# Optimization experiments

Measured on AMD Instinct MI355X. Metric: run time of the kernel, lower is better.

Reference implementation:

```python
import jax, jax.numpy as jnp
import numpy as np

B, L, D, H, C = 16, 512, 1280, 512, 5


def setup_inputs() -> dict:
    key = jax.random.key(0)
    ks = jax.random.split(key, 20)
    emb = jax.random.normal(ks[0], (B, L, D), jnp.float32)
    lengths = jax.random.randint(ks[1], (B,), 16, L + 1)
    attention_mask = (jnp.arange(L)[None, :] < lengths[:, None]).astype(jnp.int32)
    sc = 1.0 / np.sqrt(H)
    u = lambda k, s: jax.random.uniform(k, s, jnp.float32, -sc, sc)
    return dict(
        embeddings=emb,
        attention_mask=attention_mask,
        h0=jax.random.normal(ks[2], (2, B, H), jnp.float32),
        c0=jax.random.normal(ks[3], (2, B, H), jnp.float32),
        w_ih_f=u(ks[4], (4 * H, D)), w_hh_f=u(ks[5], (4 * H, H)),
        b_ih_f=u(ks[6], (4 * H,)), b_hh_f=u(ks[7], (4 * H,)),
        w_ih_b=u(ks[8], (4 * H, D)), w_hh_b=u(ks[9], (4 * H, H)),
        b_ih_b=u(ks[10], (4 * H,)), b_hh_b=u(ks[11], (4 * H,)),
        w_out=u(ks[12], (2 * H, C)), b_out=u(ks[13], (C,)),
        crf_start=jax.random.normal(ks[14], (C,), jnp.float32) * 0.1,
        crf_end=jax.random.normal(ks[15], (C,), jnp.float32) * 0.1,
        crf_trans=jax.random.normal(ks[16], (C, C), jnp.float32) * 0.1,
    )


def _lstm_dir(x, h0, c0, w_ih, w_hh, b_ih, b_hh):
    # x: [B, T, D] -> hidden states [B, T, H]; PyTorch gate order (i, f, g, o)
    xg = jnp.einsum('btd,gd->btg', x, w_ih) + b_ih + b_hh  # [B, T, 4H]

    def step(carry, xw_t):
        h, c = carry
        g = xw_t + h @ w_hh.T
        i, f, gg, o = jnp.split(g, 4, axis=-1)
        c = jax.nn.sigmoid(f) * c + jax.nn.sigmoid(i) * jnp.tanh(gg)
        h = jax.nn.sigmoid(o) * jnp.tanh(c)
        return (h, c), h

    _, hs = jax.lax.scan(step, (h0, c0), xg.transpose(1, 0, 2))
    return hs.transpose(1, 0, 2)


def _emissions(embeddings, attention_mask, h0, c0, w_ih_f, w_hh_f, b_ih_f, b_hh_f,
               w_ih_b, w_hh_b, b_ih_b, b_hh_b, w_out, b_out):
    lengths = attention_mask.sum(axis=1)
    x = embeddings[:, 1:-1]                                   # drop CLS position, shift left
    Tp = x.shape[1]
    valid = jnp.arange(Tp)[None, :] < (lengths - 2)[:, None]  # remove_cls crop [1:len-1], left-aligned pad
    x = jnp.where(valid[:, :, None], x, 0.0)
    hf = _lstm_dir(x, h0[0], c0[0], w_ih_f, w_hh_f, b_ih_f, b_hh_f)
    hb = _lstm_dir(x[:, ::-1], h0[1], c0[1], w_ih_b, w_hh_b, b_ih_b, b_hh_b)[:, ::-1]
    h = jnp.concatenate([hf, hb], axis=-1)                    # [B, Tp, 2H]
    return h @ w_out + b_out, valid


def _viterbi_decode(emissions, mask, start, end, trans):
    Bn, Tp, Ct = emissions.shape
    ident = jnp.arange(Ct, dtype=jnp.int32)
    score0 = start[None, :] + emissions[:, 0]                 # [B, C]

    def step(score, inp):
        emit_t, m_t = inp                                      # [B, C], [B]
        br = score[:, :, None] + trans[None] + emit_t[:, None, :]
        ns = br.max(axis=1)
        idx = br.argmax(axis=1).astype(jnp.int32)
        idx = jnp.where(m_t[:, None], idx, ident[None, :])     # identity backpointer past seq end
        score = jnp.where(m_t[:, None], ns, score)
        return score, idx

    score, hist = jax.lax.scan(step, score0,
                               (emissions[:, 1:].transpose(1, 0, 2), mask[:, 1:].T))
    score = score + end[None, :]
    last = jnp.argmax(score, axis=-1).astype(jnp.int32)        # [B]
    bidx = jnp.arange(Bn)

    def bstep(tag, idx_t):
        prev = idx_t[bidx, tag]
        return prev, prev

    _, prevs = jax.lax.scan(bstep, last, hist, reverse=True)   # [Tp-1, B]
    tags = jnp.concatenate([prevs, last[None, :]], axis=0).transpose(1, 0)
    return tags


def reference(embeddings, attention_mask, h0, c0, w_ih_f, w_hh_f, b_ih_f, b_hh_f,
              w_ih_b, w_hh_b, b_ih_b, b_hh_b, w_out, b_out, crf_start, crf_end, crf_trans):
    emissions, valid = _emissions(embeddings, attention_mask, h0, c0,
                                  w_ih_f, w_hh_f, b_ih_f, b_hh_f,
                                  w_ih_b, w_hh_b, b_ih_b, b_hh_b, w_out, b_out)
    tags = _viterbi_decode(emissions, valid, crf_start, crf_end, crf_trans)
    return tags, valid  # tags valid where mask True (past-end entries repeat last tag)
```

## Files before the change

kernel.cpp:

```cpp
#include <hip/hip_runtime.h>

typedef unsigned short u16;
typedef unsigned int u32;
typedef __bf16 bf16x8 __attribute__((ext_vector_type(8)));
typedef u16 u16x8 __attribute__((ext_vector_type(8)));
typedef float f32x4 __attribute__((ext_vector_type(4)));
typedef u32 u32x2 __attribute__((ext_vector_type(2)));
typedef u32 u32x4 __attribute__((ext_vector_type(4)));

#define B_ 16
#define T_ 510
#define H_ 512
#define N_ 4096
#define KSPLIT 2560

#define OFF_ABIG  0ull
#define OFF_BBIG  41943040ull
#define OFF_BIAS  62914560ull
#define OFF_XG    62930944ull
#define OFF_HS    197148672ull
#define OFF_EMIS  230572032ull
#define OFF_V     230735232ull
#define OFF_FLAGS 230735296ull
#define OFF_PROBE  (OFF_EMIS + 131328ull)
#define OFF_CTRL   (OFF_EMIS + 131584ull)
#define CHUNKA_OFF 0ull
#define CHUNKB_OFF 262144ull

#define MAGIC_ 0x5EC0FFEE
#define POLL_BUDGET 65536
#define ARB_BUDGET  262144

#define GL_LDS(g, s) __builtin_amdgcn_global_load_lds(                      \
    (const __attribute__((address_space(1))) void*)(g),                     \
    (__attribute__((address_space(3))) void*)(s), 16, 0, 0)

__device__ __forceinline__ u16 f2bf(float x) {
  u32 u = __float_as_uint(x);
  u32 r = (u + 0x7fffu + ((u >> 16) & 1u)) >> 16;
  return (u16)r;
}
__device__ __forceinline__ float bf2f(u16 h) { return __uint_as_float(((u32)h) << 16); }

__device__ __forceinline__ int ld_cc(const int* p) {
  int f;
  asm volatile("global_load_dword %0, %1, off sc0 sc1\n\ts_waitcnt vmcnt(0)" : "=v"(f) : "v"(p) : "memory");
  return f;
}
__device__ __forceinline__ void st_cc(int* p, int v) {
  asm volatile("global_store_dword %0, %1, off sc0 sc1\n\ts_waitcnt vmcnt(0)" :: "v"(p), "v"(v) : "memory");
}

__device__ __forceinline__ float sigm_f(float x) {
  float e = __expf(-x);
  return __builtin_amdgcn_rcpf(1.f + e);
}
__device__ __forceinline__ float tanh_f(float x) {
  float e = __expf(2.f * x);
  return 1.f - 2.f * __builtin_amdgcn_rcpf(e + 1.f);
}

__global__ __launch_bounds__(256) void k_prep(const int* __restrict__ mask, int* __restrict__ V,
                                              int* __restrict__ flagsA, int* __restrict__ probe,
                                              int* __restrict__ ctrl) {
  __shared__ int red[4];
  int b = blockIdx.x, tid = threadIdx.x;
  int s = mask[b * 512 + tid] + mask[b * 512 + 256 + tid];
  for (int off = 32; off; off >>= 1) s += __shfl_down(s, off);
  if ((tid & 63) == 0) red[tid >> 6] = s;
  __syncthreads();
  if (tid == 0) V[b] = red[0] + red[1] + red[2] + red[3] - 2;
  if (b == 0 && tid < 64) flagsA[tid] = 0;
  if (b == 3 && tid < 64) probe[tid] = 0;
  if (b == 1 && tid < 16) ctrl[tid] = 0;
}

__global__ __launch_bounds__(256) void k_zero(char* __restrict__ p) {
  u32x4 z = (u32x4){0u, 0u, 0u, 0u};
  char* dst = p + ((size_t)blockIdx.x * 256 + threadIdx.x) * 16;
  asm volatile("global_store_dwordx4 %0, %1, off sc0 sc1" :: "v"(dst), "v"(z) : "memory");
}

__global__ __launch_bounds__(256) void k_valid(const int* __restrict__ V, int* __restrict__ out) {
  int idx = blockIdx.x * 256 + threadIdx.x;
  if (idx < B_ * T_) {
    int b = idx / T_, t = idx - b * T_;
    out[B_ * T_ + idx] = (t < V[b]) ? 1 : 0;
  }
}

__global__ __launch_bounds__(320) void k_splitA(const float* __restrict__ emb, const int* __restrict__ V,
                                                u16* __restrict__ Abig) {
  int row = blockIdx.x;
  int k0 = threadIdx.x * 4;
  u16* dst = Abig + (size_t)row * KSPLIT;
  float4 v = {0.f, 0.f, 0.f, 0.f};
  if (row < B_ * T_) {
    int b = row / T_, t = row - b * T_;
    if (t < V[b]) v = *(const float4*)(emb + (size_t)(b * 512 + t + 1) * 1280 + k0);
  }
  float vs[4] = {v.x, v.y, v.z, v.w};
  ushort4 hi, lo;
  u16 h0_ = f2bf(vs[0]); u16 l0_ = f2bf(vs[0] - bf2f(h0_));
  u16 h1_ = f2bf(vs[1]); u16 l1_ = f2bf(vs[1] - bf2f(h1_));
  u16 h2_ = f2bf(vs[2]); u16 l2_ = f2bf(vs[2] - bf2f(h2_));
  u16 h3_ = f2bf(vs[3]); u16 l3_ = f2bf(vs[3] - bf2f(h3_));
  hi.x = h0_; hi.y = h1_; hi.z = h2_; hi.w = h3_;
  lo.x = l0_; lo.y = l1_; lo.z = l2_; lo.w = l3_;
  *(ushort4*)(dst + k0) = hi;
  *(ushort4*)(dst + 1280 + k0) = lo;
}

__global__ __launch_bounds__(320) void k_splitB(const float* __restrict__ wf, const float* __restrict__ wb,
                                                const float* __restrict__ bihf, const float* __restrict__ bhhf,
                                                const float* __restrict__ bihb, const float* __restrict__ bhhb,
                                                u16* __restrict__ Bbig, float* __restrict__ bias) {
  int n = blockIdx.x;
  int k0 = threadIdx.x * 4;
  int d = n >> 11, g = n & 2047;
  const float* w = (d ? wb : wf) + (size_t)g * 1280;
  float4 v = *(const float4*)(w + k0);
  float vs[4] = {v.x, v.y, v.z, v.w};
  ushort4 hi, lo;
  u16 h0_ = f2bf(vs[0]); u16 l0_ = f2bf(vs[0] - bf2f(h0_));
  u16 h1_ = f2bf(vs[1]); u16 l1_ = f2bf(vs[1] - bf2f(h1_));
  u16 h2_ = f2bf(vs[2]); u16 l2_ = f2bf(vs[2] - bf2f(h2_));
  u16 h3_ = f2bf(vs[3]); u16 l3_ = f2bf(vs[3] - bf2f(h3_));
  hi.x = h0_; hi.y = h1_; hi.z = h2_; hi.w = h3_;
  lo.x = l0_; lo.y = l1_; lo.z = l2_; lo.w = l3_;
  u16* dst = Bbig + (size_t)n * KSPLIT;
  *(ushort4*)(dst + k0) = hi;
  *(ushort4*)(dst + 1280 + k0) = lo;
  if (threadIdx.x == 0) bias[n] = d ? (bihb[g] + bhhb[g]) : (bihf[g] + bhhf[g]);
}

__global__ __launch_bounds__(256, 2) void k_gemm(const u16* __restrict__ A, const u16* __restrict__ Bt,
                                                 const float* __restrict__ bias, float* __restrict__ C) {
  __shared__ __align__(16) u16 As[128 * 64];
  __shared__ __align__(16) u16 Bs[128 * 64];
  const int tid = threadIdx.x;
  const int w = tid >> 6, l = tid & 63;
  const int wm = w >> 1, wn = w & 1;
  const int bm = blockIdx.x, bn = blockIdx.y;
  f32x4 acc[4][4];
#pragma unroll
  for (int m = 0; m < 4; ++m)
#pragma unroll
    for (int n = 0; n < 4; ++n) acc[m][n] = (f32x4){0.f, 0.f, 0.f, 0.f};

  const int rQ = tid >> 3;
  const int cB = (tid & 7) * 16;
  const char* gA = (const char*)(A + (size_t)(bm * 128) * KSPLIT) + cB;
  const char* gB = (const char*)(Bt + (size_t)(bn * 128) * KSPLIT) + cB;

  for (int kt = 0; kt < 60; ++kt) {
    const int s = kt / 20, ks = kt - s * 20;
    const int aOff = ((s == 2) ? 1280 : 0) + ks * 64;
    const int bOff = ((s == 1) ? 1280 : 0) + ks * 64;
    __syncthreads();
#pragma unroll
    for (int q = 0; q < 4; ++q) {
      GL_LDS(gA + ((size_t)(q * 32 + rQ) * KSPLIT + aOff) * 2, (char*)As + q * 4096 + tid * 16);
      GL_LDS(gB + ((size_t)(q * 32 + rQ) * KSPLIT + bOff) * 2, (char*)Bs + q * 4096 + tid * 16);
    }
    __syncthreads();
#pragma unroll
    for (int kc = 0; kc < 2; ++kc) {
      bf16x8 af[4], bfr[4];
      const int kByte = kc * 64 + (l >> 4) * 16;
#pragma unroll
      for (int m = 0; m < 4; ++m)
        af[m] = *(const bf16x8*)((const char*)As + (wm * 64 + m * 16 + (l & 15)) * 128 + kByte);
#pragma unroll
      for (int n = 0; n < 4; ++n)
        bfr[n] = *(const bf16x8*)((const char*)Bs + (wn * 64 + n * 16 + (l & 15)) * 128 + kByte);
#pragma unroll
      for (int m = 0; m < 4; ++m)
#pragma unroll
        for (int n = 0; n < 4; ++n)
          acc[m][n] = __builtin_amdgcn_mfma_f32_16x16x32_bf16(af[m], bfr[n], acc[m][n], 0, 0, 0);
    }
  }
#pragma unroll
  for (int n = 0; n < 4; ++n) {
    const int gc = bn * 128 + wn * 64 + n * 16 + (l & 15);
    const float bv = bias[gc];
#pragma unroll
    for (int m = 0; m < 4; ++m) {
      const int gr0 = bm * 128 + wm * 64 + m * 16 + (l >> 4) * 4;
#pragma unroll
      for (int r = 0; r < 4; ++r) C[(size_t)(gr0 + r) * N_ + gc] = acc[m][n][r] + bv;
    }
  }
}

template <int COH>
__device__ __forceinline__ void emit_chunks(char* buf, int sub, u32 gen, const u16* pack) {
  const int tid = threadIdx.x;
  if (tid < 128) {
    const int sb = tid >> 3, r = tid & 7, p = r >> 2, j = r & 3;
    const u32* pw = (const u32*)(pack + p * 256 + sb * 16 + j * 4);
    u32x4 val;
    val[0] = pw[0]; val[1] = pw[1]; val[2] = gen; val[3] = 0u;
    char* dst = buf + sb * 4096 + p * 2048 + (sub * 4 + j) * 16;
    if constexpr (COH)
      asm volatile("global_store_dwordx4 %0, %1, off" :: "v"(dst), "v"(val) : "memory");
    else
      asm volatile("global_store_dwordx4 %0, %1, off sc0 sc1" :: "v"(dst), "v"(val) : "memory");
  }
}

template <int COH>
__device__ void run_recur(int dir, int sub, const float* __restrict__ xg, const float* __restrict__ whh,
                          const float* __restrict__ h0, const float* __restrict__ c0,
                          float* __restrict__ hs, char* __restrict__ cb,
                          u16* lds_a, float* epil, u16* pack) {
  const int tid = threadIdx.x;
  const int w = tid >> 6, l = tid & 63;
  const int c = l & 15, kg = l >> 4;
  const int gate = c >> 2, uloc = c & 3;
  const int ug = sub * 16 + w * 4 + uloc;

  __syncthreads();

  bf16x8 whi[16], wlo[16];
  {
    const float* wrow = whh + (size_t)(gate * 512 + ug) * 512 + kg * 8;
#pragma unroll
    for (int kc = 0; kc < 16; ++kc) {
      float4 v0 = *(const float4*)(wrow + kc * 32);
      float4 v1 = *(const float4*)(wrow + kc * 32 + 4);
      float vs[8] = {v0.x, v0.y, v0.z, v0.w, v1.x, v1.y, v1.z, v1.w};
      u16x8 hi, lo;
#pragma unroll
      for (int j = 0; j < 8; ++j) {
        u16 h = f2bf(vs[j]);
        hi[j] = h;
        lo[j] = f2bf(vs[j] - bf2f(h));
      }
      whi[kc] = __builtin_bit_cast(bf16x8, hi);
      wlo[kc] = __builtin_bit_cast(bf16x8, lo);
    }
  }

  const int sb = tid >> 4, su = tid & 15;
  const int gu = sub * 16 + su;
  float creg = c0[(dir * 16 + sb) * 512 + gu];
  {
    float h = h0[(dir * 16 + sb) * 512 + gu];
    u16 hh = f2bf(h), hl = f2bf(h - bf2f(hh));
    pack[sb * 16 + su] = hh;
    pack[256 + sb * 16 + su] = hl;
  }
  __syncthreads();
  emit_chunks<COH>(cb + 65536, sub, 1u, pack);

  for (int t = 0; t < T_; ++t) {
    const int trow = dir ? (T_ - 1 - t) : t;
    const u32 gen = (u32)(t + 1);
    const char* sbuf = cb + ((t + 1) & 1) * 65536;

    u32x4 v[16];
#pragma unroll
    for (int i = 0; i < 16; ++i) {
      const char* p = sbuf + ((size_t)(tid + 256 * i)) * 16;
      asm volatile("global_load_dwordx4 %0, %1, off sc0 sc1" : "=v"(v[i]) : "v"(p) : "memory");
    }
    float xv[4];
#pragma unroll
    for (int g = 0; g < 4; ++g) {
      const float* p = xg + (size_t)(sb * T_ + trow) * N_ + dir * 2048 + g * 512 + gu;
      asm volatile("global_load_dword %0, %1, off" : "=v"(xv[g]) : "v"(p) : "memory");
    }
    asm volatile("s_waitcnt vmcnt(4)" ::: "memory");
    __builtin_amdgcn_sched_barrier(0);
    while (true) {
      u32 bad = 0;
#pragma unroll
      for (int i = 0; i < 16; ++i) bad |= (v[i][2] != gen) ? (1u << i) : 0u;
      if (!bad) break;
#pragma unroll
      for (int i = 0; i < 16; ++i)
        if (bad & (1u << i)) {
          const char* p = sbuf + ((size_t)(tid + 256 * i)) * 16;
          asm volatile("global_load_dwordx4 %0, %1, off sc0 sc1" : "=v"(v[i]) : "v"(p) : "memory");
        }
      asm volatile("s_waitcnt vmcnt(0)" ::: "memory");
      __builtin_amdgcn_sched_barrier(0);
    }
#pragma unroll
    for (int i = 0; i < 16; ++i) {
      int ci = tid + 256 * i;
      int b = ci >> 8, pl = (ci >> 7) & 1, k = ci & 127;
      int off = pl * 16384 + b * 1024 + ((k * 8) ^ ((b & 7) << 4));
      *(u32x2*)((char*)lds_a + off) = (u32x2){v[i][0], v[i][1]};
    }
    __syncthreads();

    f32x4 a0 = (f32x4){0.f, 0.f, 0.f, 0.f}, a1 = a0, a2 = a0, a3 = a0, a4 = a0, a5 = a0;
#pragma unroll
    for (int kc = 0; kc < 16; ++kc) {
      const int rowb = l & 15;
      const int koff = (kc * 64 + kg * 16) ^ ((rowb & 7) << 4);
      bf16x8 ahi = *(const bf16x8*)((const char*)lds_a + rowb * 1024 + koff);
      bf16x8 alo = *(const bf16x8*)((const char*)lds_a + 16384 + rowb * 1024 + koff);
      if (kc & 1) {
        a3 = __builtin_amdgcn_mfma_f32_16x16x32_bf16(ahi, whi[kc], a3, 0, 0, 0);
        a4 = __builtin_amdgcn_mfma_f32_16x16x32_bf16(ahi, wlo[kc], a4, 0, 0, 0);
        a5 = __builtin_amdgcn_mfma_f32_16x16x32_bf16(alo, whi[kc], a5, 0, 0, 0);
      } else {
        a0 = __builtin_amdgcn_mfma_f32_16x16x32_bf16(ahi, whi[kc], a0, 0, 0, 0);
        a1 = __builtin_amdgcn_mfma_f32_16x16x32_bf16(ahi, wlo[kc], a1, 0, 0, 0);
        a2 = __builtin_amdgcn_mfma_f32_16x16x32_bf16(alo, whi[kc], a2, 0, 0, 0);
      }
    }
    f32x4 acc = ((a0 + a3) + (a1 + a4)) + (a2 + a5);

#pragma unroll
    for (int r = 0; r < 4; ++r) epil[w * 280 + (kg * 4 + r) * 17 + c] = acc[r];
    __syncthreads();
    asm volatile("s_waitcnt vmcnt(0)" ::: "memory");
    __builtin_amdgcn_sched_barrier(0);
    const int ew = su >> 2, ec = su & 3;
    const float gi = epil[ew * 280 + sb * 17 + 0 + ec] + xv[0];
    const float gf = epil[ew * 280 + sb * 17 + 4 + ec] + xv[1];
    const float gg = epil[ew * 280 + sb * 17 + 8 + ec] + xv[2];
    const float go = epil[ew * 280 + sb * 17 + 12 + ec] + xv[3];
    const float si = sigm_f(gi);
    const float sf = sigm_f(gf);
    const float so = sigm_f(go);
    const float tg = tanh_f(gg);
    creg = sf * creg + si * tg;
    const float h = so * tanh_f(creg);
    {
      u16 hh = f2bf(h), hl = f2bf(h - bf2f(hh));
      pack[sb * 16 + su] = hh;
      pack[256 + sb * 16 + su] = hl;
    }
    __syncthreads();
    emit_chunks<COH>(cb + (t & 1) * 65536, sub, (u32)(t + 2), pack);
    hs[(size_t)((dir * 16 + sb) * T_ + trow) * 512 + gu] = h;
  }
}

__global__ __launch_bounds__(256, 1) void k_recur(const float* __restrict__ xg, const float* __restrict__ whh_f,
                                                  const float* __restrict__ whh_b, const float* __restrict__ h0,
                                                  const float* __restrict__ c0, float* __restrict__ hs,
                                                  char* __restrict__ chunkA, char* __restrict__ chunkB,
                                                  int* __restrict__ flagsA, int* __restrict__ probe,
                                                  int* __restrict__ ctrl) {
  __shared__ __align__(16) u16 lds_a[16384];
  __shared__ float epil[4 * 280];
  __shared__ u16 pack[512];
  __shared__ int s_act, s_cfg;

  const int tid = threadIdx.x;

  if (tid == 0) {
    int xcc;
    asm volatile("s_getreg_b32 %0, hwreg(HW_REG_XCC_ID)" : "=s"(xcc));
    xcc &= 7;
    int slot = 99;
    if (xcc < 2) slot = __hip_atomic_fetch_add(&ctrl[4 + xcc], 1, __ATOMIC_RELAXED, __HIP_MEMORY_SCOPE_AGENT);
    const int roleA = (xcc < 2 && slot < 32);
    const int dir = xcc, sub = slot;

    if (roleA) {
      int mg = MAGIC_;
      asm volatile("global_store_dword %0, %1, off\n\ts_waitcnt vmcnt(0)" :: "v"(probe + dir * 32 + sub), "v"(mg) : "memory");
      st_cc(flagsA + dir * 32 + sub, 2);
      bool complete = false;
      for (int it = 0; it < POLL_BUDGET && !complete; ++it) {
        complete = true;
        for (int j = 0; j < 32; ++j)
          if (ld_cc(flagsA + dir * 32 + j) < 2) { complete = false; break; }
        if (!complete) __builtin_amdgcn_s_sleep(16);
      }
      int myval = 99;
      if (complete) {
        bool ok = true;
        for (int j = 0; j < 32; ++j)
          if (ld_cc(probe + dir * 32 + j) != MAGIC_) { ok = false; break; }
        if (ok) myval = 3;
      }
      st_cc(flagsA + dir * 32 + sub, myval);
      if (sub == 0) {
        bool go = false;
        for (int it = 0; it < POLL_BUDGET; ++it) {
          int n3 = 0; bool bad = false;
          for (int j = 0; j < 32; ++j) {
            int f = ld_cc(flagsA + dir * 32 + j);
            if (f == 99) { bad = true; break; }
            if (f == 3) ++n3;
          }
          if (bad) break;
          if (n3 == 32) { go = true; break; }
          __builtin_amdgcn_s_sleep(16);
        }
        st_cc(&ctrl[12 + dir], go ? 1 : 2);
      }
    }

    if (blockIdx.x == 0) {
      int v0 = 0, v1 = 0;
      for (int it = 0; it < ARB_BUDGET; ++it) {
        v0 = ld_cc(&ctrl[12]);
        v1 = ld_cc(&ctrl[13]);
        if (v0 && v1) break;
        __builtin_amdgcn_s_sleep(16);
      }
      st_cc(&ctrl[14], 4 | (v0 == 1 ? 1 : 0) | (v1 == 1 ? 2 : 0));
    }

    int cfg;
    do {
      cfg = ld_cc(&ctrl[14]);
      if (!cfg) __builtin_amdgcn_s_sleep(16);
    } while (!cfg);

    s_cfg = cfg;
    s_act = (roleA && (cfg & (1 << dir))) ? (dir | (sub << 1)) : -1;
  }
  __syncthreads();
  const int act = s_act, cfg = s_cfg;

  if (act >= 0) {
    const int adir = act & 1, asub = act >> 1;
    run_recur<1>(adir, asub, xg, adir ? whh_b : whh_f, h0, c0, hs,
                 chunkA + adir * 131072, lds_a, epil, pack);
  }
  if (blockIdx.x < 64) {
    const int mdir = (int)blockIdx.x >> 5, msub = (int)blockIdx.x & 31;
    if (!(cfg & (1 << mdir)))
      run_recur<0>(mdir, msub, xg, mdir ? whh_b : whh_f, h0, c0, hs,
                   chunkB + mdir * 131072, lds_a, epil, pack);
  }
}

__global__ __launch_bounds__(256) void k_emis(const float* __restrict__ hs, const float* __restrict__ wout,
                                              const float* __restrict__ bout, float* __restrict__ e) {
  const int tid = threadIdx.x;
  const int w = tid >> 6, l = tid & 63;
  const int row = blockIdx.x * 4 + w;
  const int b = row / T_, t = row - b * T_;
  const float* hf = hs + (size_t)(b * T_ + t) * 512;
  const float* hb = hs + (size_t)((16 + b) * T_ + t) * 512;
  float a0 = 0, a1 = 0, a2 = 0, a3 = 0, a4 = 0;
#pragma unroll
  for (int it = 0; it < 8; ++it) {
    int u = it * 64 + l;
    float hv = hf[u];
    const float* wr = wout + u * 5;
    a0 += hv * wr[0]; a1 += hv * wr[1]; a2 += hv * wr[2]; a3 += hv * wr[3]; a4 += hv * wr[4];
  }
#pragma unroll
  for (int it = 0; it < 8; ++it) {
    int u = it * 64 + l;
    float hv = hb[u];
    const float* wr = wout + (512 + u) * 5;
    a0 += hv * wr[0]; a1 += hv * wr[1]; a2 += hv * wr[2]; a3 += hv * wr[3]; a4 += hv * wr[4];
  }
  for (int off = 32; off; off >>= 1) {
    a0 += __shfl_down(a0, off);
    a1 += __shfl_down(a1, off);
    a2 += __shfl_down(a2, off);
    a3 += __shfl_down(a3, off);
    a4 += __shfl_down(a4, off);
  }
  if (l == 0) {
    float* ep = e + (size_t)row * 5;
    ep[0] = a0 + bout[0];
    ep[1] = a1 + bout[1];
    ep[2] = a2 + bout[2];
    ep[3] = a3 + bout[3];
    ep[4] = a4 + bout[4];
  }
}

__global__ __launch_bounds__(64) void k_viterbi(const float* __restrict__ e, const int* __restrict__ V,
                                                const float* __restrict__ start, const float* __restrict__ endv,
                                                const float* __restrict__ trans, int* __restrict__ out) {
  __shared__ float els[T_ * 5];
  __shared__ unsigned char hist[(T_ - 1) * 5];
  __shared__ float strans[25];
  const int b = blockIdx.x, l = threadIdx.x;
  for (int i = l; i < T_ * 5; i += 64) els[i] = e[(size_t)b * T_ * 5 + i];
  if (l < 25) strans[l] = trans[l];
  const int Vb = V[b];
  __syncthreads();
  const int cl = (l < 5) ? l : 0;
  float score = (l < 5) ? (start[l] + els[l]) : -1e30f;
  for (int t = 1; t < T_; ++t) {
    const bool valid = t < Vb;
    float m = -1e30f;
    int arg = 0;
#pragma unroll
    for (int p = 0; p < 5; ++p) {
      float v = __shfl(score, p) + strans[p * 5 + cl];
      if (v > m) { m = v; arg = p; }
    }
    if (l < 5) {
      if (valid) {
        score = m + els[t * 5 + l];
        hist[(t - 1) * 5 + l] = (unsigned char)arg;
      } else {
        hist[(t - 1) * 5 + l] = (unsigned char)l;
      }
    }
  }
  float sc = (l < 5) ? (score + endv[l]) : -1e30f;
  int last = 0;
  float mb = -1e30f;
#pragma unroll
  for (int p = 0; p < 5; ++p) {
    float v = __shfl(sc, p);
    if (v > mb) { mb = v; last = p; }
  }
  __syncthreads();
  if (l == 0) {
    int tag = last;
    out[b * T_ + (T_ - 1)] = tag;
    for (int t = T_ - 2; t >= 0; --t) {
      tag = hist[t * 5 + tag];
      out[b * T_ + t] = tag;
    }
  }
}

extern "C" void kernel_launch(void* const* d_in, const int* in_sizes, int n_in, void* d_out, int out_size,
                              void* d_ws, size_t ws_size, hipStream_t stream) {
  const float* emb = (const float*)d_in[0];
  const int* amask = (const int*)d_in[1];
  const float* h0 = (const float*)d_in[2];
  const float* c0 = (const float*)d_in[3];
  const float* wihf = (const float*)d_in[4];
  const float* whhf = (const float*)d_in[5];
  const float* bihf = (const float*)d_in[6];
  const float* bhhf = (const float*)d_in[7];
  const float* wihb = (const float*)d_in[8];
  const float* whhb = (const float*)d_in[9];
  const float* bihb = (const float*)d_in[10];
  const float* bhhb = (const float*)d_in[11];
  const float* wout = (const float*)d_in[12];
  const float* bout = (const float*)d_in[13];
  const float* cstart = (const float*)d_in[14];
  const float* cend = (const float*)d_in[15];
  const float* ctrans = (const float*)d_in[16];

  char* ws = (char*)d_ws;
  u16* Abig = (u16*)(ws + OFF_ABIG);
  u16* Bbig = (u16*)(ws + OFF_BBIG);
  float* bias = (float*)(ws + OFF_BIAS);
  float* xg = (float*)(ws + OFF_XG);
  float* hs = (float*)(ws + OFF_HS);
  float* emis = (float*)(ws + OFF_EMIS);
  int* V = (int*)(ws + OFF_V);
  int* flagsA = (int*)(ws + OFF_FLAGS);
  int* probe = (int*)(ws + OFF_PROBE);
  int* ctrl = (int*)(ws + OFF_CTRL);
  char* chunkA = ws + CHUNKA_OFF;
  char* chunkB = ws + CHUNKB_OFF;
  int* out = (int*)d_out;

  hipLaunchKernelGGL(k_prep, dim3(16), dim3(256), 0, stream, amask, V, flagsA, probe, ctrl);
  hipLaunchKernelGGL(k_valid, dim3(32), dim3(256), 0, stream, V, out);
  hipLaunchKernelGGL(k_splitA, dim3(8192), dim3(320), 0, stream, emb, V, Abig);
  hipLaunchKernelGGL(k_splitB, dim3(4096), dim3(320), 0, stream, wihf, wihb, bihf, bhhf, bihb, bhhb, Bbig, bias);
  hipLaunchKernelGGL(k_gemm, dim3(64, 32), dim3(256), 0, stream, Abig, Bbig, bias, xg);
  hipLaunchKernelGGL(k_zero, dim3(128), dim3(256), 0, stream, chunkA);
  hipLaunchKernelGGL(k_recur, dim3(256), dim3(256), 0, stream, xg, whhf, whhb, h0, c0, hs,
                     chunkA, chunkB, flagsA, probe, ctrl);
  hipLaunchKernelGGL(k_emis, dim3(2040), dim3(256), 0, stream, hs, wout, bout, emis);
  hipLaunchKernelGGL(k_viterbi, dim3(16), dim3(64), 0, stream, emis, V, cstart, cend, ctrans, out);
}
```

Baseline: 1.826 ms.

## Replace generation-tagged hidden-state chunks with packed payloads and per-block flags

The recurrent kernel's cross-block exchange of hidden state is reworked. Previously each 16-byte chunk carried its own generation tag and readers re-polled stale chunks. Now each block writes a compact 4-byte hi/lo bf16 payload per unit and then bumps a per-block flag. Readers poll the flags before loading half as much data. This also drops the separate zeroing kernel and the LDS pack buffer, and adds a second flag array for the fallback path. The cost is that each wave now polls its 8 flags one after another with a full wait per poll, which adds serial latency to every timestep.

New measurement: 1.969 ms. 7.8% more time.

```diff
diff --git a/kernel.cpp b/kernel.cpp
--- a/kernel.cpp
+++ b/kernel.cpp
@@ -22,6 +22,7 @@
 #define OFF_EMIS  230572032ull
 #define OFF_V     230735232ull
 #define OFF_FLAGS 230735296ull
+#define OFF_FLAGSB (OFF_EMIS + 131072ull)
 #define OFF_PROBE  (OFF_EMIS + 131328ull)
 #define OFF_CTRL   (OFF_EMIS + 131584ull)
 #define CHUNKA_OFF 0ull
@@ -50,6 +51,9 @@
 __device__ __forceinline__ void st_cc(int* p, int v) {
   asm volatile("global_store_dword %0, %1, off sc0 sc1\n\ts_waitcnt vmcnt(0)" :: "v"(p), "v"(v) : "memory");
 }
+__device__ __forceinline__ void st_plain(int* p, int v) {
+  asm volatile("global_store_dword %0, %1, off\n\ts_waitcnt vmcnt(0)" :: "v"(p), "v"(v) : "memory");
+}
 
 __device__ __forceinline__ float sigm_f(float x) {
   float e = __expf(-x);
@@ -61,8 +65,8 @@
 }
 
 __global__ __launch_bounds__(256) void k_prep(const int* __restrict__ mask, int* __restrict__ V,
-                                              int* __restrict__ flagsA, int* __restrict__ probe,
-                                              int* __restrict__ ctrl) {
+                                              int* __restrict__ flagsA, int* __restrict__ flagsB,
+                                              int* __restrict__ probe, int* __restrict__ ctrl) {
   __shared__ int red[4];
   int b = blockIdx.x, tid = threadIdx.x;
   int s = mask[b * 512 + tid] + mask[b * 512 + 256 + tid];
@@ -71,14 +75,9 @@
   __syncthreads();
   if (tid == 0) V[b] = red[0] + red[1] + red[2] + red[3] - 2;
   if (b == 0 && tid < 64) flagsA[tid] = 0;
+  if (b == 2 && tid < 64) flagsB[tid] = 0;
   if (b == 3 && tid < 64) probe[tid] = 0;
   if (b == 1 && tid < 16) ctrl[tid] = 0;
-}
-
-__global__ __launch_bounds__(256) void k_zero(char* __restrict__ p) {
-  u32x4 z = (u32x4){0u, 0u, 0u, 0u};
-  char* dst = p + ((size_t)blockIdx.x * 256 + threadIdx.x) * 16;
-  asm volatile("global_store_dwordx4 %0, %1, off sc0 sc1" :: "v"(dst), "v"(z) : "memory");
 }
 
 __global__ __launch_bounds__(256) void k_valid(const int* __restrict__ V, int* __restrict__ out) {
@@ -195,31 +194,16 @@
 }
 
 template <int COH>
-__device__ __forceinline__ void emit_chunks(char* buf, int sub, u32 gen, const u16* pack) {
-  const int tid = threadIdx.x;
-  if (tid < 128) {
-    const int sb = tid >> 3, r = tid & 7, p = r >> 2, j = r & 3;
-    const u32* pw = (const u32*)(pack + p * 256 + sb * 16 + j * 4);
-    u32x4 val;
-    val[0] = pw[0]; val[1] = pw[1]; val[2] = gen; val[3] = 0u;
-    char* dst = buf + sb * 4096 + p * 2048 + (sub * 4 + j) * 16;
-    if constexpr (COH)
-      asm volatile("global_store_dwordx4 %0, %1, off" :: "v"(dst), "v"(val) : "memory");
-    else
-      asm volatile("global_store_dwordx4 %0, %1, off sc0 sc1" :: "v"(dst), "v"(val) : "memory");
-  }
-}
-
-template <int COH>
 __device__ void run_recur(int dir, int sub, const float* __restrict__ xg, const float* __restrict__ whh,
                           const float* __restrict__ h0, const float* __restrict__ c0,
-                          float* __restrict__ hs, char* __restrict__ cb,
-                          u16* lds_a, float* epil, u16* pack) {
+                          float* __restrict__ hs, char* __restrict__ cb, int* __restrict__ flags,
+                          u16* lds_a, float* epil) {
   const int tid = threadIdx.x;
   const int w = tid >> 6, l = tid & 63;
   const int c = l & 15, kg = l >> 4;
   const int gate = c >> 2, uloc = c & 3;
   const int ug = sub * 16 + w * 4 + uloc;
+  constexpr int GB = COH ? 9 : 0;
 
   __syncthreads();
 
@@ -245,26 +229,41 @@
 
   const int sb = tid >> 4, su = tid & 15;
   const int gu = sub * 16 + su;
+  const int sbC = l >> 2, q = l & 3;
+
   float creg = c0[(dir * 16 + sb) * 512 + gu];
   {
     float h = h0[(dir * 16 + sb) * 512 + gu];
     u16 hh = f2bf(h), hl = f2bf(h - bf2f(hh));
-    pack[sb * 16 + su] = hh;
-    pack[256 + sb * 16 + su] = hl;
+    u32 pay = (u32)hh | ((u32)hl << 16);
+    int* p = (int*)(cb + 32768 + sb * 2048 + (size_t)(sub * 16 + su) * 4);
+    if constexpr (COH) st_plain(p, (int)pay);
+    else st_cc(p, (int)pay);
   }
   __syncthreads();
-  emit_chunks<COH>(cb + 65536, sub, 1u, pack);
+  if (tid == 0) {
+    if constexpr (COH) st_plain(flags + dir * 32 + sub, 1 + GB);
+    else st_cc(flags + dir * 32 + sub, 1 + GB);
+  }
 
   for (int t = 0; t < T_; ++t) {
     const int trow = dir ? (T_ - 1 - t) : t;
-    const u32 gen = (u32)(t + 1);
-    const char* sbuf = cb + ((t + 1) & 1) * 65536;
-
-    u32x4 v[16];
-#pragma unroll
-    for (int i = 0; i < 16; ++i) {
-      const char* p = sbuf + ((size_t)(tid + 256 * i)) * 16;
-      asm volatile("global_load_dwordx4 %0, %1, off sc0 sc1" : "=v"(v[i]) : "v"(p) : "memory");
+    const int gen = t + 1 + GB;
+    const char* sbuf = cb + ((t + 1) & 1) * 32768;
+
+    u32x4 vch[8];
+#pragma unroll
+    for (int jj = 0; jj < 8; ++jj) {
+      const int j = w * 8 + jj;
+      const int* fp = flags + (dir << 5) + j;
+      while (true) {
+        int f;
+        asm volatile("global_load_dword %0, %1, off sc0 sc1\n\ts_waitcnt vmcnt(0)" : "=v"(f) : "v"(fp) : "memory");
+        if (f >= gen) break;
+        if constexpr (!COH) __builtin_amdgcn_s_sleep(1);
+      }
+      const char* p = sbuf + sbC * 2048 + (size_t)(j * 16 + q * 4) * 4;
+      asm volatile("global_load_dwordx4 %0, %1, off sc0 sc1" : "=v"(vch[jj]) : "v"(p) : "memory");
     }
     float xv[4];
 #pragma unroll
@@ -272,28 +271,17 @@
       const float* p = xg + (size_t)(sb * T_ + trow) * N_ + dir * 2048 + g * 512 + gu;
       asm volatile("global_load_dword %0, %1, off" : "=v"(xv[g]) : "v"(p) : "memory");
     }
-    asm volatile("s_waitcnt vmcnt(4)" ::: "memory");
+    asm volatile("s_waitcnt vmcnt(0)" ::: "memory");
     __builtin_amdgcn_sched_barrier(0);
-    while (true) {
-      u32 bad = 0;
-#pragma unroll
-      for (int i = 0; i < 16; ++i) bad |= (v[i][2] != gen) ? (1u << i) : 0u;
-      if (!bad) break;
-#pragma unroll
-      for (int i = 0; i < 16; ++i)
-        if (bad & (1u << i)) {
-          const char* p = sbuf + ((size_t)(tid + 256 * i)) * 16;
-          asm volatile("global_load_dwordx4 %0, %1, off sc0 sc1" : "=v"(v[i]) : "v"(p) : "memory");
-        }
-      asm volatile("s_waitcnt vmcnt(0)" ::: "memory");
-      __builtin_amdgcn_sched_barrier(0);
-    }
-#pragma unroll
-    for (int i = 0; i < 16; ++i) {
-      int ci = tid + 256 * i;
-      int b = ci >> 8, pl = (ci >> 7) & 1, k = ci & 127;
-      int off = pl * 16384 + b * 1024 + ((k * 8) ^ ((b & 7) << 4));
-      *(u32x2*)((char*)lds_a + off) = (u32x2){v[i][0], v[i][1]};
+#pragma unroll
+    for (int jj = 0; jj < 8; ++jj) {
+      const int j = w * 8 + jj;
+      const u32 u0 = vch[jj][0], u1 = vch[jj][1], u2 = vch[jj][2], u3 = vch[jj][3];
+      u32x2 hi2 = (u32x2){(u0 & 0xFFFFu) | (u1 << 16), (u2 & 0xFFFFu) | (u3 << 16)};
+      u32x2 lo2 = (u32x2){(u0 >> 16) | (u1 & 0xFFFF0000u), (u2 >> 16) | (u3 & 0xFFFF0000u)};
+      const int bo = (j * 32 + q * 8) ^ ((sbC & 7) << 4);
+      *(u32x2*)((char*)lds_a + sbC * 1024 + bo) = hi2;
+      *(u32x2*)((char*)lds_a + 16384 + sbC * 1024 + bo) = lo2;
     }
     __syncthreads();
 
@@ -319,8 +307,6 @@
 #pragma unroll
     for (int r = 0; r < 4; ++r) epil[w * 280 + (kg * 4 + r) * 17 + c] = acc[r];
     __syncthreads();
-    asm volatile("s_waitcnt vmcnt(0)" ::: "memory");
-    __builtin_amdgcn_sched_barrier(0);
     const int ew = su >> 2, ec = su & 3;
     const float gi = epil[ew * 280 + sb * 17 + 0 + ec] + xv[0];
     const float gf = epil[ew * 280 + sb * 17 + 4 + ec] + xv[1];
@@ -334,11 +320,23 @@
     const float h = so * tanh_f(creg);
     {
       u16 hh = f2bf(h), hl = f2bf(h - bf2f(hh));
-      pack[sb * 16 + su] = hh;
-      pack[256 + sb * 16 + su] = hl;
+      u32 pay = (u32)hh | ((u32)hl << 16);
+      char* p = cb + (t & 1) * 32768 + sb * 2048 + (size_t)(sub * 16 + su) * 4;
+      if constexpr (COH)
+        asm volatile("global_store_dword %0, %1, off\n\ts_waitcnt vmcnt(0)" :: "v"(p), "v"(pay) : "memory");
+      else
+        asm volatile("global_store_dword %0, %1, off sc0 sc1\n\ts_waitcnt vmcnt(0)" :: "v"(p), "v"(pay) : "memory");
     }
     __syncthreads();
-    emit_chunks<COH>(cb + (t & 1) * 65536, sub, (u32)(t + 2), pack);
+    if (tid == 0) {
+      if constexpr (COH) {
+        int gv = t + 2 + GB;
+        asm volatile("global_store_dword %0, %1, off" :: "v"(flags + dir * 32 + sub), "v"(gv) : "memory");
+      } else {
+        int gv = t + 2 + GB;
+        asm volatile("global_store_dword %0, %1, off sc0 sc1" :: "v"(flags + dir * 32 + sub), "v"(gv) : "memory");
+      }
+    }
     hs[(size_t)((dir * 16 + sb) * T_ + trow) * 512 + gu] = h;
   }
 }
@@ -347,11 +345,10 @@
                                                   const float* __restrict__ whh_b, const float* __restrict__ h0,
                                                   const float* __restrict__ c0, float* __restrict__ hs,
                                                   char* __restrict__ chunkA, char* __restrict__ chunkB,
-                                                  int* __restrict__ flagsA, int* __restrict__ probe,
-                                                  int* __restrict__ ctrl) {
+                                                  int* __restrict__ flagsA, int* __restrict__ flagsB,
+                                                  int* __restrict__ probe, int* __restrict__ ctrl) {
   __shared__ __align__(16) u16 lds_a[16384];
   __shared__ float epil[4 * 280];
-  __shared__ u16 pack[512];
   __shared__ int s_act, s_cfg;
 
   const int tid = threadIdx.x;
@@ -427,13 +424,13 @@
   if (act >= 0) {
     const int adir = act & 1, asub = act >> 1;
     run_recur<1>(adir, asub, xg, adir ? whh_b : whh_f, h0, c0, hs,
-                 chunkA + adir * 131072, lds_a, epil, pack);
+                 chunkA + adir * 131072, flagsA, lds_a, epil);
   }
   if (blockIdx.x < 64) {
     const int mdir = (int)blockIdx.x >> 5, msub = (int)blockIdx.x & 31;
     if (!(cfg & (1 << mdir)))
       run_recur<0>(mdir, msub, xg, mdir ? whh_b : whh_f, h0, c0, hs,
-                   chunkB + mdir * 131072, lds_a, epil, pack);
+                   chunkB + mdir * 131072, flagsB, lds_a, epil);
   }
 }
 
@@ -556,20 +553,20 @@
   float* emis = (float*)(ws + OFF_EMIS);
   int* V = (int*)(ws + OFF_V);
   int* flagsA = (int*)(ws + OFF_FLAGS);
+  int* flagsB = (int*)(ws + OFF_FLAGSB);
   int* probe = (int*)(ws + OFF_PROBE);
   int* ctrl = (int*)(ws + OFF_CTRL);
   char* chunkA = ws + CHUNKA_OFF;
   char* chunkB = ws + CHUNKB_OFF;
   int* out = (int*)d_out;
 
-  hipLaunchKernelGGL(k_prep, dim3(16), dim3(256), 0, stream, amask, V, flagsA, probe, ctrl);
+  hipLaunchKernelGGL(k_prep, dim3(16), dim3(256), 0, stream, amask, V, flagsA, flagsB, probe, ctrl);
   hipLaunchKernelGGL(k_valid, dim3(32), dim3(256), 0, stream, V, out);
   hipLaunchKernelGGL(k_splitA, dim3(8192), dim3(320), 0, stream, emb, V, Abig);
   hipLaunchKernelGGL(k_splitB, dim3(4096), dim3(320), 0, stream, wihf, wihb, bihf, bhhf, bihb, bhhb, Bbig, bias);
   hipLaunchKernelGGL(k_gemm, dim3(64, 32), dim3(256), 0, stream, Abig, Bbig, bias, xg);
-  hipLaunchKernelGGL(k_zero, dim3(128), dim3(256), 0, stream, chunkA);
   hipLaunchKernelGGL(k_recur, dim3(256), dim3(256), 0, stream, xg, whhf, whhb, h0, c0, hs,
-                     chunkA, chunkB, flagsA, probe, ctrl);
+                     chunkA, chunkB, flagsA, flagsB, probe, ctrl);
   hipLaunchKernelGGL(k_emis, dim3(2040), dim3(256), 0, stream, hs, wout, bout, emis);
   hipLaunchKernelGGL(k_viterbi, dim3(16), dim3(64), 0, stream, emis, V, cstart, cend, ctrans, out);
 }
```
